# Optimization experiments

Hardware: AMD Instinct MI355X
Metric: run time of the kernel (lower is better)

## Reference

```python
import jax, jax.numpy as jnp
import numpy as np

EPS = 1e-7


def setup_inputs() -> dict:
    key = jax.random.key(0)
    k1, k2, k3, k4 = jax.random.split(key, 4)
    N, M = 8192, 8192
    inputs = jax.random.normal(k1, (N, 2), dtype=jnp.float32)
    outputs = jax.random.normal(k2, (N,), dtype=jnp.float32)
    x = jax.random.normal(k3, (M, 2), dtype=jnp.float32)
    # positive per-query bandwidths in [0.5, 1.5)
    bandwidth = 0.5 + jax.random.uniform(k4, (M,), dtype=jnp.float32)
    return {"x": x, "inputs": inputs, "outputs": outputs, "bandwidth": bandwidth}


def reference(x, inputs, outputs, bandwidth):
    # Squared pairwise distances (cdist followed by .pow(2) in the original):
    # d2[n, m] = ||inputs[n] - x[m]||^2, computed via the expansion to avoid
    # materializing an (N, M, 2) intermediate.
    a2 = jnp.sum(inputs * inputs, axis=1)  # (N,)
    b2 = jnp.sum(x * x, axis=1)            # (M,)
    d2 = a2[:, None] + b2[None, :] - 2.0 * (inputs @ x.T)  # (N, M)
    d2 = jnp.maximum(d2, 0.0)

    bw = bandwidth[None, :]  # (1, M), per-query bandwidth
    weights = jnp.exp(-d2 / (2.0 * bw * bw))  # (N, M)
    # Normalization over dim 0 (over the N reference points)
    weights = weights / (jnp.sum(weights, axis=0, keepdims=True) + EPS)
    # weights.T @ outputs -> (M,), Nadaraya-Watson weighted sum
    weighted = weights.T @ outputs  # (M,)
    return weighted
```

## Files before the change

### kernel.cpp

```cpp
#include <hip/hip_runtime.h>

#define EPS 1e-7f
#define LOG2E 1.44269504088896340736f

typedef float f32x2 __attribute__((ext_vector_type(2)));
typedef float f32x4 __attribute__((ext_vector_type(4)));

constexpr int BLOCK = 1024;
constexpr int JJ    = 4;
constexpr int JR    = 4;
constexpr int JB    = JJ * JR;
constexpr int SS    = BLOCK / JJ;
constexpr int CHUNK = 1024;
constexpr int PTS   = CHUNK / SS;
constexpr int ROW   = 12;
constexpr int ASZ   = SS * ROW;

__global__ __launch_bounds__(BLOCK, 2) void nw_block(
    const float2* __restrict__ x,
    const float2* __restrict__ inputs,
    const float*  __restrict__ outputs,
    const float*  __restrict__ bw,
    float*        __restrict__ out,
    int N, int M)
{
    __shared__ __align__(16) float smem[3 * ASZ];
    float* sX = smem;
    float* sY = smem + ASZ;
    float* sO = smem + 2 * ASZ;

    const int tid = threadIdx.x;
    const int jj  = tid & (JJ - 1);
    const int ss  = tid >> 2;
    const int j0  = blockIdx.x * JB;

    f32x2 c0p[JR], c1p[JR], c2p[JR], c3p[JR];
    #pragma unroll
    for (int r = 0; r < JR; ++r) {
        const int j = j0 + jj + r * JJ;
        float k = 0.f, v1 = 0.f, v2 = 0.f, v3 = 0.f;
        if (j < M) {
            float2 xj = x[j];
            float  b  = bw[j];
            k  = -LOG2E / (2.0f * b * b);
            v1 = -2.0f * k * xj.x;
            v2 = -2.0f * k * xj.y;
            v3 = k * fmaf(xj.x, xj.x, xj.y * xj.y);
        }
        c0p[r] = {k, k}; c1p[r] = {v1, v1}; c2p[r] = {v2, v2}; c3p[r] = {v3, v3};
    }

    f32x2 nump[JR], denp[JR];
    #pragma unroll
    for (int r = 0; r < JR; ++r) { nump[r] = {0.f, 0.f}; denp[r] = {0.f, 0.f}; }

    float2 pin = make_float2(0.f, 0.f);
    float  po  = 0.f;
    if (tid < N) { pin = inputs[tid]; po = outputs[tid]; }

    for (int base = 0; base < N; base += CHUNK) {
        {
            const bool v = (base + tid) < N;
            sX[ss * ROW + jj] = v ? pin.x : 1.0e19f;
            sY[ss * ROW + jj] = v ? pin.y : 0.f;
            sO[ss * ROW + jj] = v ? po    : 0.f;
        }
        __syncthreads();

        {
            const int nb = base + CHUNK;
            const int gi = nb + tid;
            if (nb < N && gi < N) { pin = inputs[gi]; po = outputs[gi]; }
        }

        {
            const f32x4 xq = *(const f32x4*)&sX[ss * ROW];
            const f32x4 yq = *(const f32x4*)&sY[ss * ROW];
            const f32x4 oq = *(const f32x4*)&sO[ss * ROW];
            const f32x2 x0 = {xq.x, xq.y}, x1 = {xq.z, xq.w};
            const f32x2 y0 = {yq.x, yq.y}, y1 = {yq.z, yq.w};
            const f32x2 o0 = {oq.x, oq.y}, o1 = {oq.z, oq.w};
            #pragma unroll
            for (int r = 0; r < JR; ++r) {
                f32x2 Aa = __builtin_elementwise_fma(c0p[r], x0, c1p[r]);
                f32x2 Ba = __builtin_elementwise_fma(c0p[r], y0, c2p[r]);
                f32x2 ta = __builtin_elementwise_fma(Ba, y0, c3p[r]);
                ta = __builtin_elementwise_fma(Aa, x0, ta);
                f32x2 Ab = __builtin_elementwise_fma(c0p[r], x1, c1p[r]);
                f32x2 Bb = __builtin_elementwise_fma(c0p[r], y1, c2p[r]);
                f32x2 tb = __builtin_elementwise_fma(Bb, y1, c3p[r]);
                tb = __builtin_elementwise_fma(Ab, x1, tb);
                f32x2 wa, wb;
                wa.x = __builtin_amdgcn_exp2f(ta.x);
                wa.y = __builtin_amdgcn_exp2f(ta.y);
                wb.x = __builtin_amdgcn_exp2f(tb.x);
                wb.y = __builtin_amdgcn_exp2f(tb.y);
                nump[r] = __builtin_elementwise_fma(wa, o0, nump[r]);
                nump[r] = __builtin_elementwise_fma(wb, o1, nump[r]);
                denp[r] += wa + wb;
            }
        }
        __syncthreads();
    }

    float2 (*red)[JB] = (float2 (*)[JB])smem;
    #pragma unroll
    for (int r = 0; r < JR; ++r)
        red[ss][jj + r * JJ] = make_float2(nump[r].x + nump[r].y,
                                           denp[r].x + denp[r].y);
    __syncthreads();
    if (tid < 16 * JB) {
        const int s2   = tid >> 4;
        const int slot = tid & (JB - 1);
        float n = 0.f, d = 0.f;
        #pragma unroll
        for (int k = 0; k < SS / 16; ++k) {
            n += red[s2 + 16 * k][slot].x;
            d += red[s2 + 16 * k][slot].y;
        }
        red[s2][slot] = make_float2(n, d);
    }
    __syncthreads();
    if (tid < JB) {
        float n = 0.f, d = 0.f;
        #pragma unroll
        for (int s = 0; s < 16; ++s) {
            n += red[s][tid].x;
            d += red[s][tid].y;
        }
        const int j = j0 + tid;
        if (j < M) out[j] = n / (d + EPS);
    }
}

extern "C" void kernel_launch(void* const* d_in, const int* in_sizes, int n_in,
                              void* d_out, int out_size, void* d_ws, size_t ws_size,
                              hipStream_t stream) {
    const float2* x       = (const float2*)d_in[0];
    const float2* inputs  = (const float2*)d_in[1];
    const float*  outputs = (const float*) d_in[2];
    const float*  bwv     = (const float*) d_in[3];
    const int N = in_sizes[2];
    const int M = in_sizes[3];
    float*        out     = (float*)d_out;

    dim3 grid((M + JB - 1) / JB);
    nw_block<<<grid, BLOCK, 0, stream>>>(x, inputs, outputs, bwv, out, N, M);
}
```

Baseline: 76.23 us.

## Precompute point squared norms in LDS and use wave shuffles for final reduction

Each thread now writes the squared norm of its reference point into a fourth shared array. The exponent is then built from three FMAs per pair (y, x, norm terms) instead of four dependent FMAs, which cuts VALU work in the inner loop. The final reduction also changes: each wave reduces with shuffles and writes one partial per wave, replacing the two-stage LDS reduction. In exchange there is an extra LDS array plus an extra load and store per chunk, and padded points now rely on a 3e38 sentinel norm to push the exponent to -inf.

```diff
diff --git a/kernel.cpp b/kernel.cpp
--- a/kernel.cpp
+++ b/kernel.cpp
@@ -14,7 +14,7 @@
 constexpr int CHUNK = 1024;
 constexpr int PTS   = CHUNK / SS;
 constexpr int ROW   = 12;
-constexpr int ASZ   = SS * ROW;
+constexpr int WAVES = BLOCK / 64;
 
 __global__ __launch_bounds__(BLOCK, 2) void nw_block(
     const float2* __restrict__ x,
@@ -24,15 +24,18 @@
     float*        __restrict__ out,
     int N, int M)
 {
-    __shared__ __align__(16) float smem[3 * ASZ];
-    float* sX = smem;
-    float* sY = smem + ASZ;
-    float* sO = smem + 2 * ASZ;
+    __shared__ __align__(16) float sX[SS][ROW];
+    __shared__ __align__(16) float sY[SS][ROW];
+    __shared__ __align__(16) float sS[SS][ROW];
+    __shared__ __align__(16) float sO[SS][ROW];
+    __shared__ float2 red[WAVES][JB];
 
-    const int tid = threadIdx.x;
-    const int jj  = tid & (JJ - 1);
-    const int ss  = tid >> 2;
-    const int j0  = blockIdx.x * JB;
+    const int tid  = threadIdx.x;
+    const int jj   = tid & (JJ - 1);
+    const int ss   = tid >> 2;
+    const int wid  = tid >> 6;
+    const int lane = tid & 63;
+    const int j0   = blockIdx.x * JB;
 
     f32x2 c0p[JR], c1p[JR], c2p[JR], c3p[JR];
     #pragma unroll
@@ -61,9 +64,10 @@
     for (int base = 0; base < N; base += CHUNK) {
         {
             const bool v = (base + tid) < N;
-            sX[ss * ROW + jj] = v ? pin.x : 1.0e19f;
-            sY[ss * ROW + jj] = v ? pin.y : 0.f;
-            sO[ss * ROW + jj] = v ? po    : 0.f;
+            sX[ss][jj] = v ? pin.x : 0.f;
+            sY[ss][jj] = v ? pin.y : 0.f;
+            sS[ss][jj] = v ? fmaf(pin.x, pin.x, pin.y * pin.y) : 3.0e38f;
+            sO[ss][jj] = v ? po    : 0.f;
         }
         __syncthreads();
 
@@ -74,22 +78,22 @@
         }
 
         {
-            const f32x4 xq = *(const f32x4*)&sX[ss * ROW];
-            const f32x4 yq = *(const f32x4*)&sY[ss * ROW];
-            const f32x4 oq = *(const f32x4*)&sO[ss * ROW];
+            const f32x4 xq = *(const f32x4*)&sX[ss][0];
+            const f32x4 yq = *(const f32x4*)&sY[ss][0];
+            const f32x4 sq = *(const f32x4*)&sS[ss][0];
+            const f32x4 oq = *(const f32x4*)&sO[ss][0];
             const f32x2 x0 = {xq.x, xq.y}, x1 = {xq.z, xq.w};
             const f32x2 y0 = {yq.x, yq.y}, y1 = {yq.z, yq.w};
+            const f32x2 s0 = {sq.x, sq.y}, s1 = {sq.z, sq.w};
             const f32x2 o0 = {oq.x, oq.y}, o1 = {oq.z, oq.w};
             #pragma unroll
             for (int r = 0; r < JR; ++r) {
-                f32x2 Aa = __builtin_elementwise_fma(c0p[r], x0, c1p[r]);
-                f32x2 Ba = __builtin_elementwise_fma(c0p[r], y0, c2p[r]);
-                f32x2 ta = __builtin_elementwise_fma(Ba, y0, c3p[r]);
-                ta = __builtin_elementwise_fma(Aa, x0, ta);
-                f32x2 Ab = __builtin_elementwise_fma(c0p[r], x1, c1p[r]);
-                f32x2 Bb = __builtin_elementwise_fma(c0p[r], y1, c2p[r]);
-                f32x2 tb = __builtin_elementwise_fma(Bb, y1, c3p[r]);
-                tb = __builtin_elementwise_fma(Ab, x1, tb);
+                f32x2 ta = __builtin_elementwise_fma(c2p[r], y0, c3p[r]);
+                ta = __builtin_elementwise_fma(c1p[r], x0, ta);
+                ta = __builtin_elementwise_fma(c0p[r], s0, ta);
+                f32x2 tb = __builtin_elementwise_fma(c2p[r], y1, c3p[r]);
+                tb = __builtin_elementwise_fma(c1p[r], x1, tb);
+                tb = __builtin_elementwise_fma(c0p[r], s1, tb);
                 f32x2 wa, wb;
                 wa.x = __builtin_amdgcn_exp2f(ta.x);
                 wa.y = __builtin_amdgcn_exp2f(ta.y);
@@ -103,30 +107,25 @@
         __syncthreads();
     }
 
-    float2 (*red)[JB] = (float2 (*)[JB])smem;
     #pragma unroll
-    for (int r = 0; r < JR; ++r)
-        red[ss][jj + r * JJ] = make_float2(nump[r].x + nump[r].y,
-                                           denp[r].x + denp[r].y);
-    __syncthreads();
-    if (tid < 16 * JB) {
-        const int s2   = tid >> 4;
-        const int slot = tid & (JB - 1);
-        float n = 0.f, d = 0.f;
+    for (int r = 0; r < JR; ++r) {
+        float n = nump[r].x + nump[r].y;
+        float d = denp[r].x + denp[r].y;
         #pragma unroll
-        for (int k = 0; k < SS / 16; ++k) {
-            n += red[s2 + 16 * k][slot].x;
-            d += red[s2 + 16 * k][slot].y;
+        for (int off = 4; off < 64; off <<= 1) {
+            n += __shfl_down(n, off);
+            d += __shfl_down(d, off);
         }
-        red[s2][slot] = make_float2(n, d);
+        if (lane < JJ)
+            red[wid][jj + r * JJ] = make_float2(n, d);
     }
     __syncthreads();
     if (tid < JB) {
         float n = 0.f, d = 0.f;
         #pragma unroll
-        for (int s = 0; s < 16; ++s) {
-            n += red[s][tid].x;
-            d += red[s][tid].y;
+        for (int w = 0; w < WAVES; ++w) {
+            n += red[w][tid].x;
+            d += red[w][tid].y;
         }
         const int j = j0 + tid;
         if (j < M) out[j] = n / (d + EPS);
```

Measured after the change: 78.97 us. 1.04x slower.
